# Performance work log

Hardware: AMD Instinct MI355X
Metric: run time of the kernel (lower is better)

The kernel has to match this reference:

```python
import jax, jax.numpy as jnp
import numpy as np

NUM_SENS_CLASS = 2   # sensitive attribute in {0,1} -> sens classes {1,2}
NEG_INF = -9e15


def fair_select(adj, sens, key):
    """Per-row class-balanced random edge dropping.
    adj: [Nd, Ns] float 0/1 adjacency; sens: [Ns] int in {1..C}.
    For each row: count neighbors per sensitive class, keep = min positive
    count, randomly drop excess edges of over-represented classes."""
    mask = adj > 0
    onehot = jax.nn.one_hot(sens - 1, NUM_SENS_CLASS, dtype=jnp.float32)  # [Ns, C]
    counts = mask.astype(jnp.float32) @ onehot                            # [Nd, C]
    keep = jnp.min(jnp.where(counts > 0, counts, jnp.inf), axis=1)        # [Nd]
    rnd = jax.random.uniform(key, adj.shape)
    drop = jnp.zeros(adj.shape, dtype=bool)
    for c in range(1, NUM_SENS_CLASS + 1):
        cls = mask & (sens[None, :] == c)
        scores = jnp.where(cls, rnd, jnp.inf)
        # rank of each edge within (row, class); non-class entries rank last
        rank = jnp.argsort(jnp.argsort(scores, axis=1), axis=1)
        drop = drop | (cls & (rank >= keep[:, None]))
    return jnp.where(drop, 0.0, adj)


def setup_inputs() -> dict:
    key = jax.random.key(0)
    ks = jax.random.split(key, 10)
    N, F, T, D, K, H = 6000, 512, 256, 64, 64, 4
    bias = jax.random.randint(ks[0], (N, N), 0, 2, dtype=jnp.int32)
    emb_dest = jax.random.normal(ks[1], (N, D), jnp.float32)
    emb_src = jax.random.normal(ks[2], (N, D), jnp.float32)
    feature_src = jax.random.normal(ks[3], (N, F), jnp.float32)
    sens_col = jax.random.randint(ks[4], (N,), 0, 2).astype(jnp.float32)
    feature_src = feature_src.at[:, -1].set(sens_col)
    # learned params (xavier-style init)
    W = jax.random.normal(ks[5], (H, D, K), jnp.float32) * (1.414 * (2.0 / (D + K)) ** 0.5)
    W2 = jax.random.normal(ks[6], (H, K, K), jnp.float32) * (1.414 * (2.0 / (K + K)) ** 0.5)
    fc_w = jax.random.normal(ks[7], (T, F), jnp.float32) * (1.414 * (2.0 / (F + T)) ** 0.5)
    fc_b = jnp.zeros((T,), jnp.float32)
    dec_w = jax.random.normal(ks[8], (F, T), jnp.float32) * (1.414 * (2.0 / (F + T)) ** 0.5)
    dec_b = jnp.zeros((F,), jnp.float32)
    return dict(bias=bias, emb_dest=emb_dest, emb_src=emb_src, feature_src=feature_src,
                W=W, W2=W2, fc_w=fc_w, fc_b=fc_b, dec_w=dec_w, dec_b=dec_b)


def reference(bias, emb_dest, emb_src, feature_src, W, W2, fc_w, fc_b, dec_w, dec_b):
    adj = bias.astype(jnp.float32)
    sens = (feature_src[:, -1] + 1.0).astype(jnp.int32)          # [Ns]
    fair_adj = fair_select(adj, sens, jax.random.key(42))        # [Nd, Ns]
    tf = feature_src @ fc_w.T + fc_b                             # [Ns, T]
    # multi-head attention attribute completion (HGNN_AC, eval mode)
    h1 = jnp.einsum('nd,hdk->hnk', emb_src, W)                   # [H, Ns, K]
    h2 = jnp.einsum('nd,hdk->hnk', emb_dest, W)                  # [H, Nd, K]
    e = jax.nn.elu(jnp.einsum('hmk,hkl,hnl->hmn', h2, W2, h1))   # [H, Nd, Ns]
    attn = jax.nn.softmax(jnp.where(fair_adj[None] > 0, e, NEG_INF), axis=-1)
    H = W.shape[0]
    feature_src_re = jnp.einsum('hmn,nt->mt', attn, tf) / H      # mean over heads
    feature_hat = tf @ dec_w.T + dec_b                           # [Ns, F]
    return feature_src_re, feature_hat
```

## Files before the change

### kernel.cpp

```cpp
#include <hip/hip_runtime.h>
#include <hip/hip_bf16.h>
#include <stdint.h>


#define N_NODES 6000
#define NPAD    6016
#define FDIM    512
#define TDIM    256
#define DDIM    64
#define NHEAD   4
#define MWORDS  94
#define NEG_SENT (-3.0e38f)

typedef unsigned int        u32;
typedef unsigned long long  u64;
typedef unsigned short      u16;
typedef __attribute__((ext_vector_type(8))) short    bf16x8;
typedef __attribute__((ext_vector_type(8))) _Float16 f16x8;
typedef __attribute__((ext_vector_type(4))) float    f32x4;

__device__ __forceinline__ u16 f2bf(float f) {
  __hip_bfloat16 h = __float2bfloat16(f);
  return *(u16*)&h;
}

__device__ __forceinline__ u32 prng_payload(u32 m, u32 j) {
  u32 flat = m * 6000u + j;
  u32 x0 = 0u, x1 = flat;
  const u32 k0 = 0u, k1 = 42u;
  const u32 k2 = 0x1BD11BDAu ^ k0 ^ k1;
  x0 += k0; x1 += k1;
#define TFR(R) { x0 += x1; x1 = (x1 << (R)) | (x1 >> (32 - (R))); x1 ^= x0; }
  TFR(13) TFR(15) TFR(26) TFR(6)
  x0 += k1; x1 += k2 + 1u;
  TFR(17) TFR(29) TFR(16) TFR(24)
  x0 += k2; x1 += k0 + 2u;
  TFR(13) TFR(15) TFR(26) TFR(6)
  x0 += k0; x1 += k1 + 3u;
  TFR(17) TFR(29) TFR(16) TFR(24)
  x0 += k1; x1 += k2 + 4u;
  TFR(13) TFR(15) TFR(26) TFR(6)
  x0 += k2; x1 += k0 + 5u;
#undef TFR
  return (x0 ^ x1) >> 9;
}

__global__ void k_prep(const float* __restrict__ fs, const float* __restrict__ fcw,
                       const float* __restrict__ decw,
                       u16* __restrict__ fs_b, u16* __restrict__ fcw_b,
                       u16* __restrict__ decw_b, u32* __restrict__ cls) {
  size_t i = (size_t)blockIdx.x * 256 + threadIdx.x;
  if (i < (size_t)NPAD * FDIM) {
    size_t n = i / FDIM;
    float v = (n < N_NODES) ? fs[(size_t)n * FDIM + (i % FDIM)] : 0.f;
    fs_b[i] = f2bf(v);
  }
  if (i < (size_t)TDIM * FDIM) fcw_b[i] = f2bf(fcw[i]);
  if (i < (size_t)FDIM * TDIM) decw_b[i] = f2bf(decw[i]);
  if (i < NPAD) cls[i] = (i < N_NODES) ? (u32)fs[i * FDIM + FDIM - 1] : 0u;
}

__global__ __launch_bounds__(256) void k_hgen(const float* __restrict__ emb_src,
                                              const float* __restrict__ emb_dest,
                                              const float* __restrict__ W,
                                              const float* __restrict__ W2,
                                              u16* __restrict__ h1f16,
                                              u16* __restrict__ g2hi, u16* __restrict__ g2lo) {
  const int n = blockIdx.x;
  const int tid = threadIdx.x;
  const int h = tid >> 6, k = tid & 63;
  const size_t oidx = ((size_t)h * NPAD + n) * DDIM + k;
  __shared__ float h2s[NHEAD][DDIM];
  if (n >= N_NODES) {
    h1f16[oidx] = 0; g2hi[oidx] = 0; g2lo[oidx] = 0;
    return;
  }
  float a1 = 0.f, a2 = 0.f;
  const float* wp = W + (size_t)h * DDIM * DDIM + k;
  const float* es = emb_src + (size_t)n * DDIM;
  const float* ed = emb_dest + (size_t)n * DDIM;
  #pragma unroll 16
  for (int d = 0; d < DDIM; ++d) {
    float w = wp[(size_t)d * DDIM];
    a1 = fmaf(es[d], w, a1);
    a2 = fmaf(ed[d], w, a2);
  }
  _Float16 hh = (_Float16)a1;
  h1f16[oidx] = *(u16*)&hh;
  h2s[h][k] = a2;
  __syncthreads();
  float g = 0.f;
  const float* w2p = W2 + (size_t)h * DDIM * DDIM + k;
  #pragma unroll 16
  for (int d = 0; d < DDIM; ++d) g = fmaf(h2s[h][d], w2p[(size_t)d * DDIM], g);
  _Float16 gh = (_Float16)g;
  _Float16 gl = (_Float16)(g - (float)gh);
  g2hi[oidx] = *(u16*)&gh;
  g2lo[oidx] = *(u16*)&gl;
}

__global__ __launch_bounds__(256) void k_gemm_tf(const u16* __restrict__ A,
                                                 const u16* __restrict__ B,
                                                 const float* __restrict__ fcb,
                                                 u16* __restrict__ tf,
                                                 u16* __restrict__ tfT) {
  const int r0 = blockIdx.x * 32;
  const int wave = threadIdx.x >> 6, lane = threadIdx.x & 63;
  const int lrow = lane & 15, lgrp = lane >> 4;
  const int n0 = wave * 64;
  f32x4 acc[2][4] = {};
  for (int ks = 0; ks < FDIM; ks += 32) {
    const int kb = ks + lgrp * 8;
    bf16x8 a[2], b[4];
    #pragma unroll
    for (int mi = 0; mi < 2; ++mi)
      a[mi] = *(const bf16x8*)(A + (size_t)(r0 + mi * 16 + lrow) * FDIM + kb);
    #pragma unroll
    for (int ni = 0; ni < 4; ++ni)
      b[ni] = *(const bf16x8*)(B + (size_t)(n0 + ni * 16 + lrow) * FDIM + kb);
    #pragma unroll
    for (int mi = 0; mi < 2; ++mi)
      #pragma unroll
      for (int ni = 0; ni < 4; ++ni)
        acc[mi][ni] = __builtin_amdgcn_mfma_f32_16x16x32_bf16(a[mi], b[ni], acc[mi][ni], 0, 0, 0);
  }
  #pragma unroll
  for (int mi = 0; mi < 2; ++mi)
    #pragma unroll
    for (int ni = 0; ni < 4; ++ni) {
      const int col = n0 + ni * 16 + lrow;
      const float bv = fcb[col];
      const int rbase = r0 + mi * 16 + lgrp * 4;
      union { u16 s[4]; uint2 v; } pk;
      #pragma unroll
      for (int q = 0; q < 4; ++q) {
        const int row = rbase + q;
        const float v = (row < N_NODES) ? (acc[mi][ni][q] + bv) : 0.f;
        const u16 hv = f2bf(v);
        tf[(size_t)row * TDIM + col] = hv;
        pk.s[q] = hv;
      }
      *(uint2*)(tfT + (size_t)col * NPAD + rbase) = pk.v;
    }
}

__global__ __launch_bounds__(256) void k_gemm_fh(const u16* __restrict__ A,
                                                 const u16* __restrict__ B,
                                                 const float* __restrict__ decb,
                                                 float* __restrict__ out1) {
  const int r0 = blockIdx.x * 32;
  const int wave = threadIdx.x >> 6, lane = threadIdx.x & 63;
  const int lrow = lane & 15, lgrp = lane >> 4;
  const int n0 = wave * 128;
  f32x4 acc[2][8] = {};
  for (int ks = 0; ks < TDIM; ks += 32) {
    const int kb = ks + lgrp * 8;
    bf16x8 a[2], b[8];
    #pragma unroll
    for (int mi = 0; mi < 2; ++mi)
      a[mi] = *(const bf16x8*)(A + (size_t)(r0 + mi * 16 + lrow) * TDIM + kb);
    #pragma unroll
    for (int ni = 0; ni < 8; ++ni)
      b[ni] = *(const bf16x8*)(B + (size_t)(n0 + ni * 16 + lrow) * TDIM + kb);
    #pragma unroll
    for (int mi = 0; mi < 2; ++mi)
      #pragma unroll
      for (int ni = 0; ni < 8; ++ni)
        acc[mi][ni] = __builtin_amdgcn_mfma_f32_16x16x32_bf16(a[mi], b[ni], acc[mi][ni], 0, 0, 0);
  }
  #pragma unroll
  for (int mi = 0; mi < 2; ++mi)
    #pragma unroll
    for (int ni = 0; ni < 8; ++ni) {
      const int col = n0 + ni * 16 + lrow;
      const float bv = decb[col];
      const int rbase = r0 + mi * 16 + lgrp * 4;
      #pragma unroll
      for (int q = 0; q < 4; ++q) {
        const int row = rbase + q;
        if (row < N_NODES) out1[(size_t)row * FDIM + col] = acc[mi][ni][q] + bv;
      }
    }
}

__global__ __launch_bounds__(256) void k_mask(const int* __restrict__ bias,
                                              const u32* __restrict__ cls,
                                              u64* __restrict__ maskbits) {
  const int m = blockIdx.x;
  const int tid = threadIdx.x;
  if (m >= N_NODES) {
    for (int t = tid; t < MWORDS; t += 256) maskbits[(size_t)m * MWORDS + t] = 0ull;
    return;
  }
  __shared__ u64 adjw[MWORDS], clsw[MWORDS], keptw[MWORDS];
  __shared__ u16 clist[NPAD];
  __shared__ u32 wordoff[MWORDS];
  __shared__ u32 hist[256];
  __shared__ u64 tkey[128];
  __shared__ u64 thrK;
  __shared__ u32 bc[4];
  __shared__ int tie_n;
  __shared__ u32 c0s, c1s;
  if (tid == 0) { tie_n = 0; c0s = 0; c1s = 0; thrK = ~0ull; }
  hist[tid] = 0u;
  __syncthreads();
  const int w = tid >> 6, lane = tid & 63;
  for (int it = 0, base = 0; base < NPAD; ++it, base += 256) {
    const int j = base + tid;
    bool adj = false, c1b = false;
    if (j < N_NODES) {
      adj = bias[(size_t)m * N_NODES + j] != 0;
      c1b = cls[j] != 0u;
    }
    const u64 ab = __ballot(adj);
    const u64 cb = __ballot(c1b);
    const int wi = it * 4 + w;
    if (lane == 0 && wi < MWORDS) { adjw[wi] = ab; clsw[wi] = cb; }
  }
  __syncthreads();
  if (tid < MWORDS) {
    const u64 a = adjw[tid], c = clsw[tid];
    const u32 n1 = (u32)__popcll(a & c);
    const u32 n0 = (u32)__popcll(a & ~c);
    if (n1) atomicAdd(&c1s, n1);
    if (n0) atomicAdd(&c0s, n0);
  }
  __syncthreads();
  const u32 c0 = c0s, c1 = c1s;
  const bool nodrop = (c0 == 0u) || (c1 == 0u) || (c0 == c1);
  if (nodrop) {
    for (int t = tid; t < MWORDS; t += 256) maskbits[(size_t)m * MWORDS + t] = adjw[t];
    return;
  }
  const bool Mis1 = (c1 > c0);
  const u32 keep = (c0 < c1) ? c0 : c1;
  const int n = Mis1 ? (int)c1 : (int)c0;
  if (tid < 64) {
    u32 cnt0w = 0;
    if (tid < MWORDS) {
      const u64 mw = adjw[tid] & (Mis1 ? clsw[tid] : ~clsw[tid]);
      cnt0w = (u32)__popcll(mw);
    }
    u32 incl = cnt0w;
    #pragma unroll
    for (int off = 1; off < 64; off <<= 1) {
      const u32 v = __shfl_up(incl, off, 64);
      if (tid >= off) incl += v;
    }
    wordoff[tid] = incl - cnt0w;
    const u32 tot0 = __shfl(incl, 63, 64);
    const int t2 = 64 + tid;
    u32 cnt1w = 0;
    if (t2 < MWORDS) {
      const u64 mw = adjw[t2] & (Mis1 ? clsw[t2] : ~clsw[t2]);
      cnt1w = (u32)__popcll(mw);
    }
    u32 incl2 = cnt1w;
    #pragma unroll
    for (int off = 1; off < 64; off <<= 1) {
      const u32 v = __shfl_up(incl2, off, 64);
      if (tid >= off) incl2 += v;
    }
    if (t2 < MWORDS) wordoff[t2] = tot0 + incl2 - cnt1w;
  }
  __syncthreads();
  for (int base = 0; base < NPAD; base += 256) {
    const int j = base + tid;
    if (j < N_NODES) {
      const int wi = j >> 6;
      const u64 mw = adjw[wi] & (Mis1 ? clsw[wi] : ~clsw[wi]);
      const u64 bitj = 1ull << (j & 63);
      if (mw & bitj) {
        const u32 rank = (u32)__popcll(mw & (bitj - 1ull));
        clist[wordoff[wi] + rank] = (u16)j;
      }
    }
  }
  __syncthreads();
  for (int i = tid; i < n; i += 256) {
    const u32 j = clist[i];
    const u32 p = prng_payload((u32)m, j);
    atomicAdd(&hist[p >> 15], 1u);
  }
  __syncthreads();
  if (tid < 64) {
    const u32 b0 = hist[tid * 4], b1 = hist[tid * 4 + 1];
    const u32 b2 = hist[tid * 4 + 2], b3 = hist[tid * 4 + 3];
    const u32 lt = b0 + b1 + b2 + b3;
    u32 incl = lt;
    #pragma unroll
    for (int off = 1; off < 64; off <<= 1) {
      const u32 v = __shfl_up(incl, off, 64);
      if (tid >= off) incl += v;
    }
    const u32 pre = incl - lt;
    if (pre < keep && keep <= incl) {
      u32 run = pre;
      u32 cc[4] = { b0, b1, b2, b3 };
      #pragma unroll
      for (int x = 0; x < 4; ++x) {
        if (run + cc[x] >= keep) { bc[0] = (u32)(tid * 4 + x); bc[1] = keep - run; break; }
        run += cc[x];
      }
    }
  }
  __syncthreads();
  const u32 bstar = bc[0], kin = bc[1];
  if (tid < MWORDS) keptw[tid] = adjw[tid] & (Mis1 ? ~clsw[tid] : clsw[tid]);
  __syncthreads();
  for (int i = tid; i < n; i += 256) {
    const u32 j = clist[i];
    const u32 p = prng_payload((u32)m, j);
    const u32 b = p >> 15;
    if (b < bstar) {
      atomicOr(&keptw[j >> 6], 1ull << (j & 63));
    } else if (b == bstar) {
      const int pos = atomicAdd(&tie_n, 1);
      if (pos < 128) tkey[pos] = ((u64)p << 13) | j;
    }
  }
  __syncthreads();
  const int cnt = tie_n < 128 ? tie_n : 128;
  if (tid < cnt) {
    const u64 me = tkey[tid];
    int smaller = 0;
    for (int s2 = 0; s2 < cnt; ++s2) smaller += (tkey[s2] < me) ? 1 : 0;
    if (smaller == (int)kin - 1) thrK = me;
  }
  __syncthreads();
  const u64 tk = thrK;
  if (tid < cnt) {
    const u64 me = tkey[tid];
    if (me <= tk) {
      const u32 j = (u32)(me & 0x1FFFu);
      atomicOr(&keptw[j >> 6], 1ull << (j & 63));
    }
  }
  __syncthreads();
  for (int t = tid; t < MWORDS; t += 256) maskbits[(size_t)m * MWORDS + t] = keptw[t];
}

__global__ __launch_bounds__(256) void k_pass1(const u16* __restrict__ g2hi, const u16* __restrict__ g2lo,
                                               const u16* __restrict__ h1f16,
                                               const u64* __restrict__ maskbits,
                                               float* __restrict__ mpart, float* __restrict__ lpart) {
  const int r0 = blockIdx.x * 64;
  const int chunk = blockIdx.y;
  const int h = blockIdx.z;
  const int c0 = chunk * 768;
  const int ntw = (chunk < 7) ? 12 : 10;
  const int wave = threadIdx.x >> 6, lane = threadIdx.x & 63;
  const int lrow = lane & 15, lgrp = lane >> 4;
  const u32 cbit = (u32)(wave * 16 + lrow);
  __shared__ float red_m[4][64], red_l[4][64];
  __shared__ u64 mk[64][12];
  {
    const int wb = chunk * 12;
    for (int i = threadIdx.x; i < 64 * 12; i += 256) {
      const int r = i / 12, wi = i % 12;
      mk[r][wi] = (wb + wi < MWORDS) ? maskbits[(size_t)(r0 + r) * MWORDS + wb + wi] : 0ull;
    }
  }
  __syncthreads();
  f16x8 ahi[4][2], alo[4][2];
  #pragma unroll
  for (int mi = 0; mi < 4; ++mi)
    #pragma unroll
    for (int ks = 0; ks < 2; ++ks) {
      const size_t off = ((size_t)h * NPAD + (r0 + mi * 16 + lrow)) * DDIM + ks * 32 + lgrp * 8;
      ahi[mi][ks] = *(const f16x8*)(g2hi + off);
      alo[mi][ks] = *(const f16x8*)(g2lo + off);
    }
  float mreg[4][4], lreg[4][4];
  #pragma unroll
  for (int mi = 0; mi < 4; ++mi)
    #pragma unroll
    for (int q = 0; q < 4; ++q) { mreg[mi][q] = NEG_SENT; lreg[mi][q] = 0.f; }
  const u16* hb = h1f16 + (size_t)h * NPAD * DDIM + lrow * DDIM + lgrp * 8;
  auto loadB = [&](f16x8* dst, int i) {
    const int ii = (i < ntw) ? i : (ntw - 1);
    const size_t off = (size_t)(c0 + (wave + 4 * ii) * 16) * DDIM;
    dst[0] = *(const f16x8*)(hb + off);
    dst[1] = *(const f16x8*)(hb + off + 32);
  };
  auto compute = [&](int i, const f16x8* b) {
    f32x4 acc[4] = {};
    #pragma unroll
    for (int ks = 0; ks < 2; ++ks)
      #pragma unroll
      for (int mi = 0; mi < 4; ++mi) {
        acc[mi] = __builtin_amdgcn_mfma_f32_16x16x32_f16(ahi[mi][ks], b[ks], acc[mi], 0, 0, 0);
        acc[mi] = __builtin_amdgcn_mfma_f32_16x16x32_f16(alo[mi][ks], b[ks], acc[mi], 0, 0, 0);
      }
    #pragma unroll
    for (int mi = 0; mi < 4; ++mi)
      #pragma unroll
      for (int q = 0; q < 4; ++q) {
        const int rowl = mi * 16 + lgrp * 4 + q;
        const bool kept = (mk[rowl][i] >> cbit) & 1ull;
        const float e = acc[mi][q];
        const float el = e > 0.f ? e : (__expf(e) - 1.f);
        const float m0 = mreg[mi][q];
        const float mn = kept ? fmaxf(m0, el) : m0;
        const float add = kept ? __expf(el - mn) : 0.f;
        lreg[mi][q] = lreg[mi][q] * __expf(m0 - mn) + add;
        mreg[mi][q] = mn;
      }
  };
  f16x8 bA[2], bB[2];
  loadB(bA, 0); loadB(bB, 1);
  for (int i = 0; i < ntw; i += 2) {
    f16x8 nA[2], nB[2];
    loadB(nA, i + 2);
    loadB(nB, i + 3);
    compute(i, bA);
    compute(i + 1, bB);
    bA[0] = nA[0]; bA[1] = nA[1];
    bB[0] = nB[0]; bB[1] = nB[1];
  }
  #pragma unroll
  for (int mi = 0; mi < 4; ++mi)
    #pragma unroll
    for (int q = 0; q < 4; ++q) {
      float m0 = mreg[mi][q], l0 = lreg[mi][q];
      #pragma unroll
      for (int s = 1; s < 16; s <<= 1) {
        const float m1 = __shfl_xor(m0, s, 64);
        const float l1 = __shfl_xor(l0, s, 64);
        const float mn = fmaxf(m0, m1);
        l0 = l0 * __expf(m0 - mn) + l1 * __expf(m1 - mn);
        m0 = mn;
      }
      mreg[mi][q] = m0; lreg[mi][q] = l0;
    }
  if (lrow == 0) {
    #pragma unroll
    for (int mi = 0; mi < 4; ++mi)
      #pragma unroll
      for (int q = 0; q < 4; ++q) {
        const int rl = mi * 16 + lgrp * 4 + q;
        red_m[wave][rl] = mreg[mi][q];
        red_l[wave][rl] = lreg[mi][q];
      }
  }
  __syncthreads();
  if (threadIdx.x < 64) {
    const int rl = threadIdx.x;
    float m0 = red_m[0][rl], l0 = red_l[0][rl];
    #pragma unroll
    for (int w2 = 1; w2 < 4; ++w2) {
      const float m1 = red_m[w2][rl], l1 = red_l[w2][rl];
      const float mn = fmaxf(m0, m1);
      l0 = l0 * __expf(m0 - mn) + l1 * __expf(m1 - mn);
      m0 = mn;
    }
    const size_t o = ((size_t)chunk * NHEAD + h) * NPAD + r0 + rl;
    mpart[o] = m0; lpart[o] = l0;
  }
}

__global__ void k_merge(const float* __restrict__ mpart, const float* __restrict__ lpart,
                        float* __restrict__ mfin, float* __restrict__ lfin) {
  const int i = blockIdx.x * 256 + threadIdx.x;
  if (i >= NHEAD * NPAD) return;
  float m0 = NEG_SENT, l0 = 0.f;
  #pragma unroll
  for (int c = 0; c < 8; ++c) {
    const float m1 = mpart[(size_t)c * (NHEAD * NPAD) + i];
    const float l1 = lpart[(size_t)c * (NHEAD * NPAD) + i];
    const float mn = fmaxf(m0, m1);
    l0 = l0 * __expf(m0 - mn) + l1 * __expf(m1 - mn);
    m0 = mn;
  }
  mfin[i] = m0; lfin[i] = l0;
}

__global__ __launch_bounds__(256) void k_pass2(const u16* __restrict__ g2hi, const u16* __restrict__ g2lo,
                                               const u16* __restrict__ h1f16,
                                               const u64* __restrict__ maskbits,
                                               const float* __restrict__ mfin, const float* __restrict__ lfin,
                                               u16* __restrict__ Amat) {
  const int r0 = blockIdx.x * 32;
  const int chunk = blockIdx.y;
  const int c0 = chunk * 256;
  const int nt = (chunk < 23) ? 16 : 8;
  const int wave = threadIdx.x >> 6, lane = threadIdx.x & 63;
  const int lrow = lane & 15, lgrp = lane >> 4;
  const u32 cbit = (u32)(wave * 16 + lrow);
  __shared__ float sm[NHEAD][32], sv[NHEAD][32], suS[32];
  __shared__ u64 mk[32][4];
  if (threadIdx.x < NHEAD * 32) {
    const int h = threadIdx.x >> 5, rl = threadIdx.x & 31;
    const float mv = mfin[(size_t)h * NPAD + r0 + rl];
    const float lv = lfin[(size_t)h * NPAD + r0 + rl];
    sm[h][rl] = mv;
    sv[h][rl] = (lv > 0.f) ? (1.f / lv) : 0.f;
  }
  if (threadIdx.x < 32) {
    float s = 0.f;
    #pragma unroll
    for (int h = 0; h < NHEAD; ++h) {
      const float lv = lfin[(size_t)h * NPAD + r0 + threadIdx.x];
      s += (lv > 0.f) ? 0.f : (1.f / 6000.f);
    }
    suS[threadIdx.x] = s;
  }
  {
    const int wb = chunk * 4;
    for (int i = threadIdx.x; i < 32 * 4; i += 256) {
      const int r = i >> 2, wi = i & 3;
      mk[r][wi] = (wb + wi < MWORDS) ? maskbits[(size_t)(r0 + r) * MWORDS + wb + wi] : 0ull;
    }
  }
  __syncthreads();
  const int ntw = nt >> 2;
  f32x4 wsum[4][2] = {};
  for (int h = 0; h < NHEAD; ++h) {
    f16x8 ahi[2][2], alo[2][2];
    #pragma unroll
    for (int mi = 0; mi < 2; ++mi)
      #pragma unroll
      for (int ks = 0; ks < 2; ++ks) {
        const size_t off = ((size_t)h * NPAD + (r0 + mi * 16 + lrow)) * DDIM + ks * 32 + lgrp * 8;
        ahi[mi][ks] = *(const f16x8*)(g2hi + off);
        alo[mi][ks] = *(const f16x8*)(g2lo + off);
      }
    const u16* hb = h1f16 + (size_t)h * NPAD * DDIM + lrow * DDIM + lgrp * 8;
    auto loadB = [&](f16x8* dst, int i) {
      const int ii = (i < ntw) ? i : (ntw - 1);
      const size_t off = (size_t)(c0 + (wave + 4 * ii) * 16) * DDIM;
      dst[0] = *(const f16x8*)(hb + off);
      dst[1] = *(const f16x8*)(hb + off + 32);
    };
    auto compute = [&](int i, const f16x8* b) {
      if (i >= ntw) return;
      f32x4 acc[2] = {};
      #pragma unroll
      for (int ks = 0; ks < 2; ++ks)
        #pragma unroll
        for (int mi = 0; mi < 2; ++mi) {
          acc[mi] = __builtin_amdgcn_mfma_f32_16x16x32_f16(ahi[mi][ks], b[ks], acc[mi], 0, 0, 0);
          acc[mi] = __builtin_amdgcn_mfma_f32_16x16x32_f16(alo[mi][ks], b[ks], acc[mi], 0, 0, 0);
        }
      #pragma unroll
      for (int mi = 0; mi < 2; ++mi)
        #pragma unroll
        for (int q = 0; q < 4; ++q) {
          const int rl = mi * 16 + lgrp * 4 + q;
          const bool kept = (mk[rl][i] >> cbit) & 1ull;
          const float v = acc[mi][q];
          const float el = v > 0.f ? v : (__expf(v) - 1.f);
          wsum[i][mi][q] += kept ? (__expf(el - sm[h][rl]) * sv[h][rl]) : 0.f;
        }
    };
    f16x8 b0[2], b1[2], b2[2], b3[2];
    loadB(b0, 0); loadB(b1, 1); loadB(b2, 2); loadB(b3, 3);
    compute(0, b0);
    compute(1, b1);
    compute(2, b2);
    compute(3, b3);
  }
  #pragma unroll
  for (int ti = 0; ti < 4; ++ti) {
    if (ti < ntw) {
      const int col = c0 + (wave + 4 * ti) * 16 + lrow;
      const float suAdd = (col < N_NODES) ? 1.f : 0.f;
      #pragma unroll
      for (int mi = 0; mi < 2; ++mi)
        #pragma unroll
        for (int q = 0; q < 4; ++q) {
          const int rl = mi * 16 + lgrp * 4 + q;
          const int row = r0 + rl;
          const float wv = wsum[ti][mi][q] + suAdd * suS[rl];
          Amat[(size_t)row * NPAD + col] = f2bf(wv);
        }
    }
  }
}

__global__ __launch_bounds__(256) void k_gemm_pv(const u16* __restrict__ Amat,
                                                 const u16* __restrict__ tfT,
                                                 float* __restrict__ out0) {
  const int r0 = blockIdx.x * 32;
  const int wave = threadIdx.x >> 6, lane = threadIdx.x & 63;
  const int lrow = lane & 15, lgrp = lane >> 4;
  const int n0 = wave * 64;
  f32x4 acc[2][4] = {};
  for (int ks = 0; ks < NPAD; ks += 32) {
    const int kb = ks + lgrp * 8;
    bf16x8 a[2], b[4];
    #pragma unroll
    for (int mi = 0; mi < 2; ++mi)
      a[mi] = *(const bf16x8*)(Amat + (size_t)(r0 + mi * 16 + lrow) * NPAD + kb);
    #pragma unroll
    for (int ni = 0; ni < 4; ++ni)
      b[ni] = *(const bf16x8*)(tfT + (size_t)(n0 + ni * 16 + lrow) * NPAD + kb);
    #pragma unroll
    for (int mi = 0; mi < 2; ++mi)
      #pragma unroll
      for (int ni = 0; ni < 4; ++ni)
        acc[mi][ni] = __builtin_amdgcn_mfma_f32_16x16x32_bf16(a[mi], b[ni], acc[mi][ni], 0, 0, 0);
  }
  #pragma unroll
  for (int mi = 0; mi < 2; ++mi)
    #pragma unroll
    for (int ni = 0; ni < 4; ++ni) {
      const int col = n0 + ni * 16 + lrow;
      const int rbase = r0 + mi * 16 + lgrp * 4;
      #pragma unroll
      for (int q = 0; q < 4; ++q) {
        const int row = rbase + q;
        if (row < N_NODES) out0[(size_t)row * TDIM + col] = acc[mi][ni][q] * 0.25f;
      }
    }
}

extern "C" void kernel_launch(void* const* d_in, const int* in_sizes, int n_in,
                              void* d_out, int out_size, void* d_ws, size_t ws_size,
                              hipStream_t stream) {
  (void)in_sizes; (void)n_in; (void)out_size; (void)ws_size;
  const int*   bias  = (const int*)  d_in[0];
  const float* emb_d = (const float*)d_in[1];
  const float* emb_s = (const float*)d_in[2];
  const float* fs    = (const float*)d_in[3];
  const float* W     = (const float*)d_in[4];
  const float* W2    = (const float*)d_in[5];
  const float* fcw   = (const float*)d_in[6];
  const float* fcb   = (const float*)d_in[7];
  const float* decw  = (const float*)d_in[8];
  const float* decb  = (const float*)d_in[9];
  float* out0 = (float*)d_out;
  float* out1 = out0 + (size_t)N_NODES * TDIM;

  char* base = (char*)d_ws;
  size_t off = 0;
  auto alloc = [&](size_t bytes) -> void* {
    off = (off + 255) & ~(size_t)255;
    void* p = base + off;
    off += bytes;
    return p;
  };
  u16*   Amat   = (u16*)  alloc((size_t)NPAD * NPAD * 2);
  u16*   tf_b   = (u16*)  alloc((size_t)NPAD * TDIM * 2);
  u16*   tfT_b  = (u16*)  alloc((size_t)TDIM * NPAD * 2);
  u16*   fs_b   = (u16*)  alloc((size_t)NPAD * FDIM * 2);
  u16*   fcw_b  = (u16*)  alloc((size_t)TDIM * FDIM * 2);
  u16*   decw_b = (u16*)  alloc((size_t)FDIM * TDIM * 2);
  u16*   h1f16  = (u16*)  alloc((size_t)NHEAD * NPAD * DDIM * 2);
  u16*   g2hi   = (u16*)  alloc((size_t)NHEAD * NPAD * DDIM * 2);
  u16*   g2lo   = (u16*)  alloc((size_t)NHEAD * NPAD * DDIM * 2);
  u64*   maskb  = (u64*)  alloc((size_t)NPAD * MWORDS * 8);
  float* mpart  = (float*)alloc((size_t)8 * NHEAD * NPAD * 4);
  float* lpart  = (float*)alloc((size_t)8 * NHEAD * NPAD * 4);
  float* mfin   = (float*)alloc((size_t)NHEAD * NPAD * 4);
  float* lfin   = (float*)alloc((size_t)NHEAD * NPAD * 4);
  u32*   cls    = (u32*)  alloc((size_t)NPAD * 4);

  hipLaunchKernelGGL(k_prep,    dim3((NPAD * FDIM) / 256), dim3(256), 0, stream,
                     fs, fcw, decw, fs_b, fcw_b, decw_b, cls);
  hipLaunchKernelGGL(k_hgen,    dim3(NPAD),                dim3(256), 0, stream,
                     emb_s, emb_d, W, W2, h1f16, g2hi, g2lo);
  hipLaunchKernelGGL(k_gemm_tf, dim3(NPAD / 32),           dim3(256), 0, stream,
                     fs_b, fcw_b, fcb, tf_b, tfT_b);
  hipLaunchKernelGGL(k_gemm_fh, dim3(NPAD / 32),           dim3(256), 0, stream,
                     tf_b, decw_b, decb, out1);
  hipLaunchKernelGGL(k_mask,    dim3(NPAD),                dim3(256), 0, stream,
                     bias, cls, maskb);
  hipLaunchKernelGGL(k_pass1,   dim3(NPAD / 64, 8, NHEAD), dim3(256), 0, stream,
                     g2hi, g2lo, h1f16, maskb, mpart, lpart);
  hipLaunchKernelGGL(k_merge,   dim3((NHEAD * NPAD) / 256),dim3(256), 0, stream,
                     mpart, lpart, mfin, lfin);
  hipLaunchKernelGGL(k_pass2,   dim3(NPAD / 32, 24),       dim3(256), 0, stream,
                     g2hi, g2lo, h1f16, maskb, mfin, lfin, Amat);
  hipLaunchKernelGGL(k_gemm_pv, dim3(NPAD / 32),           dim3(256), 0, stream,
                     Amat, tfT_b, out0);
}
```

Measured before the change: 608.4 us.

## Shrink pass2 column chunk to one mask word and double-buffer head loads

The attention-weight pass now gives each block a 64-column chunk (one mask word), launching 94 column blocks instead of 24. Each wave computes a single 16-column tile and prefetches the next head's A and B fragments into a second register buffer while the current head computes. This raises parallelism and removes the uneven tail chunk, and it lets loads overlap compute. The cost is that the g2hi/g2lo row fragments are reloaded about four times more often across blocks.

```diff
diff --git a/kernel.cpp b/kernel.cpp
--- a/kernel.cpp
+++ b/kernel.cpp
@@ -482,13 +482,13 @@
                                                u16* __restrict__ Amat) {
   const int r0 = blockIdx.x * 32;
   const int chunk = blockIdx.y;
-  const int c0 = chunk * 256;
-  const int nt = (chunk < 23) ? 16 : 8;
+  const int c0 = chunk * 64;
   const int wave = threadIdx.x >> 6, lane = threadIdx.x & 63;
   const int lrow = lane & 15, lgrp = lane >> 4;
+  const int ct = c0 + wave * 16;
   const u32 cbit = (u32)(wave * 16 + lrow);
   __shared__ float sm[NHEAD][32], sv[NHEAD][32], suS[32];
-  __shared__ u64 mk[32][4];
+  __shared__ u64 mk[32];
   if (threadIdx.x < NHEAD * 32) {
     const int h = threadIdx.x >> 5, rl = threadIdx.x & 31;
     const float mv = mfin[(size_t)h * NPAD + r0 + rl];
@@ -496,85 +496,81 @@
     sm[h][rl] = mv;
     sv[h][rl] = (lv > 0.f) ? (1.f / lv) : 0.f;
   }
-  if (threadIdx.x < 32) {
+  if (threadIdx.x >= 128 && threadIdx.x < 160) {
+    const int rl = threadIdx.x - 128;
     float s = 0.f;
     #pragma unroll
     for (int h = 0; h < NHEAD; ++h) {
-      const float lv = lfin[(size_t)h * NPAD + r0 + threadIdx.x];
+      const float lv = lfin[(size_t)h * NPAD + r0 + rl];
       s += (lv > 0.f) ? 0.f : (1.f / 6000.f);
     }
-    suS[threadIdx.x] = s;
-  }
+    suS[rl] = s;
+  }
+  if (threadIdx.x >= 192 && threadIdx.x < 224) {
+    const int rl = threadIdx.x - 192;
+    mk[rl] = maskbits[(size_t)(r0 + rl) * MWORDS + chunk];
+  }
+  __syncthreads();
+  const u16* hb = h1f16 + (size_t)(ct + lrow) * DDIM + lgrp * 8;
+  f16x8 ah[2][2][2], al[2][2][2], bb[2][2];
+  #define LOAD_AB(H, BUF)                                                            \
+    {                                                                                \
+      _Pragma("unroll")                                                              \
+      for (int mi = 0; mi < 2; ++mi)                                                 \
+        _Pragma("unroll")                                                            \
+        for (int ks = 0; ks < 2; ++ks) {                                             \
+          const size_t off = ((size_t)(H) * NPAD + (r0 + mi * 16 + lrow)) * DDIM + ks * 32 + lgrp * 8; \
+          ah[BUF][mi][ks] = *(const f16x8*)(g2hi + off);                             \
+          al[BUF][mi][ks] = *(const f16x8*)(g2lo + off);                             \
+        }                                                                            \
+      bb[BUF][0] = *(const f16x8*)(hb + (size_t)(H) * NPAD * DDIM);                  \
+      bb[BUF][1] = *(const f16x8*)(hb + (size_t)(H) * NPAD * DDIM + 32);             \
+    }
+  f32x4 wsum[2] = {};
+  LOAD_AB(0, 0)
+  #pragma unroll
+  for (int h = 0; h < NHEAD; ++h) {
+    const int cb = h & 1, nb = (h & 1) ^ 1;
+    if (h + 1 < NHEAD) {
+      if (nb == 0) LOAD_AB(h + 1, 0) else LOAD_AB(h + 1, 1)
+    }
+    f32x4 acc[2] = {};
+    #pragma unroll
+    for (int ks = 0; ks < 2; ++ks)
+      #pragma unroll
+      for (int mi = 0; mi < 2; ++mi) {
+        if (cb == 0) {
+          acc[mi] = __builtin_amdgcn_mfma_f32_16x16x32_f16(ah[0][mi][ks], bb[0][ks], acc[mi], 0, 0, 0);
+          acc[mi] = __builtin_amdgcn_mfma_f32_16x16x32_f16(al[0][mi][ks], bb[0][ks], acc[mi], 0, 0, 0);
+        } else {
+          acc[mi] = __builtin_amdgcn_mfma_f32_16x16x32_f16(ah[1][mi][ks], bb[1][ks], acc[mi], 0, 0, 0);
+          acc[mi] = __builtin_amdgcn_mfma_f32_16x16x32_f16(al[1][mi][ks], bb[1][ks], acc[mi], 0, 0, 0);
+        }
+      }
+    #pragma unroll
+    for (int mi = 0; mi < 2; ++mi)
+      #pragma unroll
+      for (int q = 0; q < 4; ++q) {
+        const int rl = mi * 16 + lgrp * 4 + q;
+        const bool kept = (mk[rl] >> cbit) & 1ull;
+        const float v = acc[mi][q];
+        const float el = v > 0.f ? v : (__expf(v) - 1.f);
+        wsum[mi][q] += kept ? (__expf(el - sm[h][rl]) * sv[h][rl]) : 0.f;
+      }
+  }
+  #undef LOAD_AB
   {
-    const int wb = chunk * 4;
-    for (int i = threadIdx.x; i < 32 * 4; i += 256) {
-      const int r = i >> 2, wi = i & 3;
-      mk[r][wi] = (wb + wi < MWORDS) ? maskbits[(size_t)(r0 + r) * MWORDS + wb + wi] : 0ull;
-    }
-  }
-  __syncthreads();
-  const int ntw = nt >> 2;
-  f32x4 wsum[4][2] = {};
-  for (int h = 0; h < NHEAD; ++h) {
-    f16x8 ahi[2][2], alo[2][2];
-    #pragma unroll
-    for (int mi = 0; mi < 2; ++mi)
-      #pragma unroll
-      for (int ks = 0; ks < 2; ++ks) {
-        const size_t off = ((size_t)h * NPAD + (r0 + mi * 16 + lrow)) * DDIM + ks * 32 + lgrp * 8;
-        ahi[mi][ks] = *(const f16x8*)(g2hi + off);
-        alo[mi][ks] = *(const f16x8*)(g2lo + off);
-      }
-    const u16* hb = h1f16 + (size_t)h * NPAD * DDIM + lrow * DDIM + lgrp * 8;
-    auto loadB = [&](f16x8* dst, int i) {
-      const int ii = (i < ntw) ? i : (ntw - 1);
-      const size_t off = (size_t)(c0 + (wave + 4 * ii) * 16) * DDIM;
-      dst[0] = *(const f16x8*)(hb + off);
-      dst[1] = *(const f16x8*)(hb + off + 32);
-    };
-    auto compute = [&](int i, const f16x8* b) {
-      if (i >= ntw) return;
-      f32x4 acc[2] = {};
-      #pragma unroll
-      for (int ks = 0; ks < 2; ++ks)
-        #pragma unroll
-        for (int mi = 0; mi < 2; ++mi) {
-          acc[mi] = __builtin_amdgcn_mfma_f32_16x16x32_f16(ahi[mi][ks], b[ks], acc[mi], 0, 0, 0);
-          acc[mi] = __builtin_amdgcn_mfma_f32_16x16x32_f16(alo[mi][ks], b[ks], acc[mi], 0, 0, 0);
-        }
-      #pragma unroll
-      for (int mi = 0; mi < 2; ++mi)
-        #pragma unroll
-        for (int q = 0; q < 4; ++q) {
-          const int rl = mi * 16 + lgrp * 4 + q;
-          const bool kept = (mk[rl][i] >> cbit) & 1ull;
-          const float v = acc[mi][q];
-          const float el = v > 0.f ? v : (__expf(v) - 1.f);
-          wsum[i][mi][q] += kept ? (__expf(el - sm[h][rl]) * sv[h][rl]) : 0.f;
-        }
-    };
-    f16x8 b0[2], b1[2], b2[2], b3[2];
-    loadB(b0, 0); loadB(b1, 1); loadB(b2, 2); loadB(b3, 3);
-    compute(0, b0);
-    compute(1, b1);
-    compute(2, b2);
-    compute(3, b3);
-  }
-  #pragma unroll
-  for (int ti = 0; ti < 4; ++ti) {
-    if (ti < ntw) {
-      const int col = c0 + (wave + 4 * ti) * 16 + lrow;
-      const float suAdd = (col < N_NODES) ? 1.f : 0.f;
-      #pragma unroll
-      for (int mi = 0; mi < 2; ++mi)
-        #pragma unroll
-        for (int q = 0; q < 4; ++q) {
-          const int rl = mi * 16 + lgrp * 4 + q;
-          const int row = r0 + rl;
-          const float wv = wsum[ti][mi][q] + suAdd * suS[rl];
-          Amat[(size_t)row * NPAD + col] = f2bf(wv);
-        }
-    }
+    const int col = ct + lrow;
+    const float suAdd = (col < N_NODES) ? 1.f : 0.f;
+    #pragma unroll
+    for (int mi = 0; mi < 2; ++mi)
+      #pragma unroll
+      for (int q = 0; q < 4; ++q) {
+        const int rl = mi * 16 + lgrp * 4 + q;
+        const int row = r0 + rl;
+        const float wv = wsum[mi][q] + suAdd * suS[rl];
+        Amat[(size_t)row * NPAD + col] = f2bf(wv);
+      }
   }
 }
 
@@ -670,7 +666,7 @@
                      g2hi, g2lo, h1f16, maskb, mpart, lpart);
   hipLaunchKernelGGL(k_merge,   dim3((NHEAD * NPAD) / 256),dim3(256), 0, stream,
                      mpart, lpart, mfin, lfin);
-  hipLaunchKernelGGL(k_pass2,   dim3(NPAD / 32, 24),       dim3(256), 0, stream,
+  hipLaunchKernelGGL(k_pass2,   dim3(NPAD / 32, MWORDS),   dim3(256), 0, stream,
                      g2hi, g2lo, h1f16, maskb, mfin, lfin, Amat);
   hipLaunchKernelGGL(k_gemm_pv, dim3(NPAD / 32),           dim3(256), 0, stream,
                      Amat, tfT_b, out0);
```

After: 773.4 us. 1.27x slower.
